# Performance work log

Hardware: AMD Instinct MI355X
Metric: run time of the kernel (lower is better)

The kernel has to match this reference:

```python
import jax, jax.numpy as jnp
import numpy as np

# task -> non-background class ids, padded with -1 to fixed width 3
NBG = np.array([[0, 1, 2], [0, 3, 4], [0, 5, 6], [0, 7, 8],
                [0, 9, -1], [0, 10, -1], [0, 11, -1]], dtype=np.int32)
NEG = -1e9      # pad logit (finite stand-in for -inf, grad-safe)
SMOOTH = 1e-5
NUM_CLASSES = 12


def setup_inputs() -> dict:
    key = jax.random.key(0)
    k1, k2, k3 = jax.random.split(key, 3)
    B, C, D, H, W = 4, 12, 32, 128, 128
    inputs = jax.random.normal(k1, (B, C, D, H, W), dtype=jnp.float32)
    task_id = jax.random.randint(k2, (B,), 0, 7, dtype=jnp.int32)
    # build targets consistent with each sample's task: labels in task_nbg[task]
    raw = jax.random.randint(k3, (B, D, H, W), 0, 3, dtype=jnp.int32)
    nbg = jnp.asarray(NBG)
    ids = nbg[task_id]                                   # [B,3]
    valid_max = jnp.where(ids[:, 2] < 0, 1, 2)           # 2-class tasks: raw in {0,1}
    raw = jnp.minimum(raw, valid_max[:, None, None, None])
    targets = jnp.take_along_axis(ids, raw.reshape(B, -1), axis=1).reshape(B, D, H, W)
    return {"inputs": inputs, "targets": targets, "task_id": task_id}


def reference(inputs, targets, task_id):
    B = inputs.shape[0]
    probs = jax.nn.softmax(inputs, axis=1)               # [B,12,D,H,W]
    nbg = jnp.asarray(NBG)
    ids = nbg[task_id]                                   # [B,3]
    mask = (ids >= 0)                                    # [B,3]
    idsc = jnp.maximum(ids, 0)
    mask5 = mask[:, :, None, None, None]
    gathered = jnp.take_along_axis(probs, idsc[:, :, None, None, None], axis=1)  # [B,3,D,H,W]
    score = jnp.where(mask5, gathered, 0.0)

    # --- remapped marginal targets: labels > 0 shifted by delta ---
    t = task_id.astype(jnp.int32)
    delta = jnp.where(t <= 4, -2 * t, -t - 4)
    tm = jnp.where(targets > 0, targets + delta[:, None, None, None], targets)   # in {0,1,2}

    # --- marginal CE: log_softmax over gathered probs (note: probs, not logits, matching torch F.cross_entropy on softmaxed inputs) ---
    logits = jnp.where(mask5, gathered, NEG)
    logp = jax.nn.log_softmax(logits, axis=1)
    nll = -jnp.take_along_axis(logp, tm[:, None], axis=1)[:, 0]                  # [B,D,H,W]
    loss_marg_ce = nll.mean(axis=(1, 2, 3)).sum() / B

    # --- marginal dice (padded classes contribute exactly 0) ---
    tgt = ((targets[:, None] == idsc[:, :, None, None, None]) & mask5).astype(probs.dtype)
    inter = jnp.sum(score * tgt, axis=(2, 3, 4))
    y_sum = jnp.sum(tgt, axis=(2, 3, 4))                 # tgt is binary: tgt*tgt == tgt
    z_sum = jnp.sum(score * score, axis=(2, 3, 4))
    dice = (2 * inter + SMOOTH) / (z_sum + y_sum + SMOOTH)
    loss_marg_dice = (1.0 - dice).sum() / B

    # --- exclusion: target_e = 1 - onehot(targets, 0..11), class 0 zeroed ---
    cls = jnp.arange(NUM_CLASSES, dtype=targets.dtype)[None, :, None, None, None]
    onehot = (targets[:, None] == cls).astype(probs.dtype)
    te = 1.0 - onehot
    te = te.at[:, 0].set(0.0)
    inter_e = jnp.sum(probs * te, axis=(2, 3, 4))
    y_e = jnp.sum(te, axis=(2, 3, 4))
    z_e = jnp.sum(probs * probs, axis=(2, 3, 4))
    dice_e = (2 * inter_e + SMOOTH) / (z_e + y_e + SMOOTH)
    loss_exc_dice = dice_e.sum() / B                     # inv=True: sum of dice scores

    loss_exc_ce = (jnp.log1p(probs) * te).mean(axis=(2, 3, 4)).sum() / B

    return (loss_marg_dice, loss_marg_ce, loss_exc_dice, loss_exc_ce)
```

## Files before the change

### kernel.cpp

```cpp
#include <hip/hip_runtime.h>


#define S4 131072
#define BLOCKS_PER_B 256
#define THREADS 256
#define NVOX 524288.0f
#define SMOOTH 1e-5f
#define L2E 1.4426950408889634f
#define LN2 0.6931471805599453f

__global__ void zero_acc(float* __restrict__ acc) {
  acc[blockIdx.x * 256 + threadIdx.x] = 0.f;
}

#define TAIL(CM) {                                                             \
  const int tv = tg.CM;                                                        \
  const bool t0 = (tv == 0), t1 = (tv == id1), t2 = (tv == id2);               \
  c1f += t1 ? 1.f : 0.f;  c2f += t2 ? 1.f : 0.f;                               \
  p0S += t0 ? g0.CM : 0.f; p1S += t1 ? g1.CM : 0.f; p2S += t2 ? g2.CM : 0.f;   \
  const float pt = t1 ? g1.CM : (t2 ? g2.CM : 0.f);                            \
  cesE2 += __builtin_amdgcn_logf(prod.CM * __builtin_amdgcn_rcpf(1.f + pt));   \
  const float s3 = __builtin_amdgcn_exp2f(g0.CM * L2E)                         \
                 + __builtin_amdgcn_exp2f(g1.CM * L2E)                         \
                 + __builtin_amdgcn_exp2f(g2.CM * L2E);                        \
  const float gt = t0 ? g0.CM : (t1 ? g1.CM : g2.CM);                          \
  ces2 += __builtin_amdgcn_logf(s3) - gt * L2E;                               \
}

__global__ __launch_bounds__(THREADS, 4)
void marg_main(const float4* __restrict__ inp, const int4* __restrict__ tgtp,
               const int* __restrict__ task_id, float* __restrict__ acc) {
  const int b   = blockIdx.x / BLOCKS_PER_B;
  const int blk = blockIdx.x % BLOCKS_PER_B;
  const int t   = task_id[b];
  const int id1 = (t <= 4) ? 2*t + 1 : t + 5;
  const int id2 = (t <= 3) ? 2*t + 2 : -1;
  const bool v2 = (id2 >= 0);

  const float4* inB = inp  + (size_t)b * 12 * S4;
  const int4*   tgB = tgtp + (size_t)b * S4;

  float aZ[12], aP[12];
  #pragma unroll
  for (int c = 0; c < 12; ++c) { aZ[c] = 0.f; aP[c] = 0.f; }
  float ces2=0.f, cesE2=0.f, c1f=0.f, c2f=0.f, p0S=0.f, p1S=0.f, p2S=0.f;

  #pragma unroll 1
  for (int it = 0; it < 2; ++it) {
    const int s = (blk * 2 + it) * THREADS + (int)threadIdx.x;
    float4 e[12];
    #pragma unroll
    for (int c = 0; c < 12; ++c) e[c] = inB[c * S4 + s];
    const int4 tg = tgB[s];

    #pragma unroll
    for (int c = 0; c < 12; ++c) {
      e[c].x = __builtin_amdgcn_exp2f(e[c].x * L2E);
      e[c].y = __builtin_amdgcn_exp2f(e[c].y * L2E);
      e[c].z = __builtin_amdgcn_exp2f(e[c].z * L2E);
      e[c].w = __builtin_amdgcn_exp2f(e[c].w * L2E);
    }
    float4 es = e[0];
    #pragma unroll
    for (int c = 1; c < 12; ++c) {
      es.x += e[c].x; es.y += e[c].y; es.z += e[c].z; es.w += e[c].w;
    }
    float4 r;
    r.x = __builtin_amdgcn_rcpf(es.x); r.y = __builtin_amdgcn_rcpf(es.y);
    r.z = __builtin_amdgcn_rcpf(es.z); r.w = __builtin_amdgcn_rcpf(es.w);

    float4 prod = make_float4(1.f, 1.f, 1.f, 1.f);
    #pragma unroll
    for (int c = 0; c < 12; ++c) {
      float4 p;
      p.x = e[c].x * r.x; p.y = e[c].y * r.y;
      p.z = e[c].z * r.z; p.w = e[c].w * r.w;
      aZ[c] += (p.x*p.x + p.y*p.y) + (p.z*p.z + p.w*p.w);
      aP[c] += (p.x + p.y) + (p.z + p.w);
      if (c > 0) {
        prod.x = fmaf(prod.x, p.x, prod.x);
        prod.y = fmaf(prod.y, p.y, prod.y);
        prod.z = fmaf(prod.z, p.z, prod.z);
        prod.w = fmaf(prod.w, p.w, prod.w);
      }
    }

    float4 ge1, ge2;
    switch (id1) {
      case 1:  ge1 = e[1];  break;  case 3:  ge1 = e[3];  break;
      case 5:  ge1 = e[5];  break;  case 7:  ge1 = e[7];  break;
      case 9:  ge1 = e[9];  break;  case 10: ge1 = e[10]; break;
      default: ge1 = e[11]; break;
    }
    switch (id2) {
      case 2:  ge2 = e[2];  break;  case 4:  ge2 = e[4];  break;
      case 6:  ge2 = e[6];  break;  case 8:  ge2 = e[8];  break;
      default: ge2 = make_float4(0.f, 0.f, 0.f, 0.f); break;
    }
    float4 g0, g1, g2;
    g0.x = e[0].x * r.x; g0.y = e[0].y * r.y; g0.z = e[0].z * r.z; g0.w = e[0].w * r.w;
    g1.x = ge1.x * r.x;  g1.y = ge1.y * r.y;  g1.z = ge1.z * r.z;  g1.w = ge1.w * r.w;
    g2.x = v2 ? ge2.x * r.x : -1e30f;  g2.y = v2 ? ge2.y * r.y : -1e30f;
    g2.z = v2 ? ge2.z * r.z : -1e30f;  g2.w = v2 ? ge2.w * r.w : -1e30f;

    TAIL(x); TAIL(y); TAIL(z); TAIL(w);
  }

  float vals[32];
  #pragma unroll
  for (int c = 0; c < 12; ++c) { vals[c] = aZ[c]; vals[12 + c] = aP[c]; }
  vals[24] = ces2; vals[25] = cesE2; vals[26] = c1f; vals[27] = c2f;
  vals[28] = p0S;  vals[29] = p1S;   vals[30] = p2S; vals[31] = 0.f;

  __shared__ float red[32][257];
  #pragma unroll
  for (int v = 0; v < 32; ++v) red[v][threadIdx.x] = vals[v];
  __syncthreads();

  const int val = threadIdx.x & 31;
  const int seg = threadIdx.x >> 5;
  const float* row = red[val];
  float ssum = 0.f;
  #pragma unroll
  for (int k = 0; k < 32; ++k) ssum += row[seg * 32 + k];
  ssum += __shfl_down(ssum, 32);
  if ((threadIdx.x & 63) < 32)
    atomicAdd(acc + (((b * 32 + val)) << 4), ssum);
}

__global__ void finalize(const float* __restrict__ acc,
                         const int* __restrict__ task_id,
                         float* __restrict__ out) {
  if (threadIdx.x != 0) return;
  float lmd = 0.f, lmce = 0.f, led = 0.f, lece = 0.f;
  for (int b = 0; b < 4; ++b) {
    const int t   = task_id[b];
    const int id1 = (t <= 4) ? 2*t + 1 : t + 5;
    const int id2 = (t <= 3) ? 2*t + 2 : -1;
    #define A(v) acc[((b * 32 + (v))) << 4]

    lmce += A(24) * LN2 / NVOX;
    lece += A(25) * LN2 / NVOX;

    const float c1 = A(26), c2 = A(27);
    const float y0 = NVOX - c1 - c2;
    const float d0 = (2.f*A(28) + SMOOTH) / (A(0)   + y0 + SMOOTH);
    const float d1 = (2.f*A(29) + SMOOTH) / (A(id1) + c1 + SMOOTH);
    float d2 = 1.f;
    if (id2 >= 0)
      d2 = (2.f*A(30) + SMOOTH) / (A(id2) + c2 + SMOOTH);
    lmd += (1.f - d0) + (1.f - d1) + (1.f - d2);

    led += SMOOTH / (A(0) + SMOOTH);
    for (int c = 1; c < 12; ++c) {
      const float ptc  = (c == id1) ? A(29) : ((c == id2) ? A(30) : 0.f);
      const float cntc = (c == id1) ? c1    : ((c == id2) ? c2    : 0.f);
      const float inter = A(12 + c) - ptc;
      const float ye    = NVOX - cntc;
      led += (2.f*inter + SMOOTH) / (A(c) + ye + SMOOTH);
    }
    #undef A
  }
  out[0] = lmd  * 0.25f;
  out[1] = lmce * 0.25f;
  out[2] = led  * 0.25f;
  out[3] = lece * 0.25f;
}

extern "C" void kernel_launch(void* const* d_in, const int* in_sizes, int n_in,
                              void* d_out, int out_size, void* d_ws, size_t ws_size,
                              hipStream_t stream) {
  const float* inputs  = (const float*)d_in[0];
  const int*   targets = (const int*)d_in[1];
  const int*   task_id = (const int*)d_in[2];
  float* out = (float*)d_out;
  float* acc = (float*)d_ws;

  zero_acc<<<dim3(8), 256, 0, stream>>>(acc);
  marg_main<<<dim3(4 * BLOCKS_PER_B), THREADS, 0, stream>>>(
      (const float4*)inputs, (const int4*)targets, task_id, acc);
  finalize<<<1, 64, 0, stream>>>(acc, task_id, out);
}
```

Baseline: 199.1 us.

## Issue both iterations' loads up front and reduce via wave shuffles

```diff
diff --git a/kernel.cpp b/kernel.cpp
--- a/kernel.cpp
+++ b/kernel.cpp
@@ -8,6 +8,10 @@
 #define SMOOTH 1e-5f
 #define L2E 1.4426950408889634f
 #define LN2 0.6931471805599453f
+
+#define WRED(v) { v += __shfl_down(v,32); v += __shfl_down(v,16); \
+                  v += __shfl_down(v,8);  v += __shfl_down(v,4);  \
+                  v += __shfl_down(v,2);  v += __shfl_down(v,1); }
 
 __global__ void zero_acc(float* __restrict__ acc) {
   acc[blockIdx.x * 256 + threadIdx.x] = 0.f;
@@ -24,10 +28,56 @@
                  + __builtin_amdgcn_exp2f(g1.CM * L2E)                         \
                  + __builtin_amdgcn_exp2f(g2.CM * L2E);                        \
   const float gt = t0 ? g0.CM : (t1 ? g1.CM : g2.CM);                          \
-  ces2 += __builtin_amdgcn_logf(s3) - gt * L2E;                               \
+  ces2 += __builtin_amdgcn_logf(s3) - gt * L2E;                                \
 }
 
-__global__ __launch_bounds__(THREADS, 4)
+#define COMPUTE(E, GE1, GE2, TG) {                                             \
+  _Pragma("unroll")                                                            \
+  for (int c = 0; c < 12; ++c) {                                               \
+    E[c].x = __builtin_amdgcn_exp2f(E[c].x * L2E);                             \
+    E[c].y = __builtin_amdgcn_exp2f(E[c].y * L2E);                             \
+    E[c].z = __builtin_amdgcn_exp2f(E[c].z * L2E);                             \
+    E[c].w = __builtin_amdgcn_exp2f(E[c].w * L2E);                             \
+  }                                                                            \
+  float4 es = E[0];                                                            \
+  _Pragma("unroll")                                                            \
+  for (int c = 1; c < 12; ++c) {                                               \
+    es.x += E[c].x; es.y += E[c].y; es.z += E[c].z; es.w += E[c].w;            \
+  }                                                                            \
+  float4 r;                                                                    \
+  r.x = __builtin_amdgcn_rcpf(es.x); r.y = __builtin_amdgcn_rcpf(es.y);        \
+  r.z = __builtin_amdgcn_rcpf(es.z); r.w = __builtin_amdgcn_rcpf(es.w);        \
+  float4 prod = make_float4(1.f, 1.f, 1.f, 1.f);                               \
+  _Pragma("unroll")                                                            \
+  for (int c = 0; c < 12; ++c) {                                               \
+    float4 p;                                                                  \
+    p.x = E[c].x * r.x; p.y = E[c].y * r.y;                                    \
+    p.z = E[c].z * r.z; p.w = E[c].w * r.w;                                    \
+    aZ[c] += (p.x*p.x + p.y*p.y) + (p.z*p.z + p.w*p.w);                        \
+    aP[c] += (p.x + p.y) + (p.z + p.w);                                        \
+    if (c > 0) {                                                               \
+      prod.x = fmaf(prod.x, p.x, prod.x);                                      \
+      prod.y = fmaf(prod.y, p.y, prod.y);                                      \
+      prod.z = fmaf(prod.z, p.z, prod.z);                                      \
+      prod.w = fmaf(prod.w, p.w, prod.w);                                      \
+    }                                                                          \
+  }                                                                            \
+  float4 g0, g1, g2;                                                           \
+  g0.x = E[0].x * r.x; g0.y = E[0].y * r.y;                                    \
+  g0.z = E[0].z * r.z; g0.w = E[0].w * r.w;                                    \
+  g1.x = __builtin_amdgcn_exp2f(GE1.x * L2E) * r.x;                            \
+  g1.y = __builtin_amdgcn_exp2f(GE1.y * L2E) * r.y;                            \
+  g1.z = __builtin_amdgcn_exp2f(GE1.z * L2E) * r.z;                            \
+  g1.w = __builtin_amdgcn_exp2f(GE1.w * L2E) * r.w;                            \
+  g2.x = v2 ? __builtin_amdgcn_exp2f(GE2.x * L2E) * r.x : -1e30f;              \
+  g2.y = v2 ? __builtin_amdgcn_exp2f(GE2.y * L2E) * r.y : -1e30f;              \
+  g2.z = v2 ? __builtin_amdgcn_exp2f(GE2.z * L2E) * r.z : -1e30f;              \
+  g2.w = v2 ? __builtin_amdgcn_exp2f(GE2.w * L2E) * r.w : -1e30f;              \
+  const int4 tg = TG;                                                          \
+  TAIL(x); TAIL(y); TAIL(z); TAIL(w);                                          \
+}
+
+__global__ __launch_bounds__(THREADS, 2)
 void marg_main(const float4* __restrict__ inp, const int4* __restrict__ tgtp,
                const int* __restrict__ task_id, float* __restrict__ acc) {
   const int b   = blockIdx.x / BLOCKS_PER_B;
@@ -36,6 +86,7 @@
   const int id1 = (t <= 4) ? 2*t + 1 : t + 5;
   const int id2 = (t <= 3) ? 2*t + 2 : -1;
   const bool v2 = (id2 >= 0);
+  const int id2c = v2 ? id2 : 0;
 
   const float4* inB = inp  + (size_t)b * 12 * S4;
   const int4*   tgB = tgtp + (size_t)b * S4;
@@ -45,87 +96,45 @@
   for (int c = 0; c < 12; ++c) { aZ[c] = 0.f; aP[c] = 0.f; }
   float ces2=0.f, cesE2=0.f, c1f=0.f, c2f=0.f, p0S=0.f, p1S=0.f, p2S=0.f;
 
-  #pragma unroll 1
-  for (int it = 0; it < 2; ++it) {
-    const int s = (blk * 2 + it) * THREADS + (int)threadIdx.x;
-    float4 e[12];
+  const int s0 = blk * (2 * THREADS) + (int)threadIdx.x;
+  const int s1 = s0 + THREADS;
+
+  float4 xa[12], xb[12];
+  #pragma unroll
+  for (int c = 0; c < 12; ++c) xa[c] = inB[(size_t)c * S4 + s0];
+  float4 ga1 = inB[(size_t)id1 * S4 + s0];
+  float4 ga2 = inB[(size_t)id2c * S4 + s0];
+  const int4 ta = tgB[s0];
+  #pragma unroll
+  for (int c = 0; c < 12; ++c) xb[c] = inB[(size_t)c * S4 + s1];
+  float4 gb1 = inB[(size_t)id1 * S4 + s1];
+  float4 gb2 = inB[(size_t)id2c * S4 + s1];
+  const int4 tb = tgB[s1];
+
+  COMPUTE(xa, ga1, ga2, ta);
+  COMPUTE(xb, gb1, gb2, tb);
+
+  WRED(ces2); WRED(cesE2); WRED(c1f); WRED(c2f);
+  WRED(p0S);  WRED(p1S);   WRED(p2S);
+  #pragma unroll
+  for (int c = 0; c < 12; ++c) { WRED(aZ[c]); WRED(aP[c]); }
+
+  __shared__ float red[4][32];
+  const int lane = threadIdx.x & 63;
+  const int wv   = threadIdx.x >> 6;
+  if (lane == 0) {
+    float* rw = red[wv];
     #pragma unroll
-    for (int c = 0; c < 12; ++c) e[c] = inB[c * S4 + s];
-    const int4 tg = tgB[s];
-
-    #pragma unroll
-    for (int c = 0; c < 12; ++c) {
-      e[c].x = __builtin_amdgcn_exp2f(e[c].x * L2E);
-      e[c].y = __builtin_amdgcn_exp2f(e[c].y * L2E);
-      e[c].z = __builtin_amdgcn_exp2f(e[c].z * L2E);
-      e[c].w = __builtin_amdgcn_exp2f(e[c].w * L2E);
-    }
-    float4 es = e[0];
-    #pragma unroll
-    for (int c = 1; c < 12; ++c) {
-      es.x += e[c].x; es.y += e[c].y; es.z += e[c].z; es.w += e[c].w;
-    }
-    float4 r;
-    r.x = __builtin_amdgcn_rcpf(es.x); r.y = __builtin_amdgcn_rcpf(es.y);
-    r.z = __builtin_amdgcn_rcpf(es.z); r.w = __builtin_amdgcn_rcpf(es.w);
-
-    float4 prod = make_float4(1.f, 1.f, 1.f, 1.f);
-    #pragma unroll
-    for (int c = 0; c < 12; ++c) {
-      float4 p;
-      p.x = e[c].x * r.x; p.y = e[c].y * r.y;
-      p.z = e[c].z * r.z; p.w = e[c].w * r.w;
-      aZ[c] += (p.x*p.x + p.y*p.y) + (p.z*p.z + p.w*p.w);
-      aP[c] += (p.x + p.y) + (p.z + p.w);
-      if (c > 0) {
-        prod.x = fmaf(prod.x, p.x, prod.x);
-        prod.y = fmaf(prod.y, p.y, prod.y);
-        prod.z = fmaf(prod.z, p.z, prod.z);
-        prod.w = fmaf(prod.w, p.w, prod.w);
-      }
-    }
-
-    float4 ge1, ge2;
-    switch (id1) {
-      case 1:  ge1 = e[1];  break;  case 3:  ge1 = e[3];  break;
-      case 5:  ge1 = e[5];  break;  case 7:  ge1 = e[7];  break;
-      case 9:  ge1 = e[9];  break;  case 10: ge1 = e[10]; break;
-      default: ge1 = e[11]; break;
-    }
-    switch (id2) {
-      case 2:  ge2 = e[2];  break;  case 4:  ge2 = e[4];  break;
-      case 6:  ge2 = e[6];  break;  case 8:  ge2 = e[8];  break;
-      default: ge2 = make_float4(0.f, 0.f, 0.f, 0.f); break;
-    }
-    float4 g0, g1, g2;
-    g0.x = e[0].x * r.x; g0.y = e[0].y * r.y; g0.z = e[0].z * r.z; g0.w = e[0].w * r.w;
-    g1.x = ge1.x * r.x;  g1.y = ge1.y * r.y;  g1.z = ge1.z * r.z;  g1.w = ge1.w * r.w;
-    g2.x = v2 ? ge2.x * r.x : -1e30f;  g2.y = v2 ? ge2.y * r.y : -1e30f;
-    g2.z = v2 ? ge2.z * r.z : -1e30f;  g2.w = v2 ? ge2.w * r.w : -1e30f;
-
-    TAIL(x); TAIL(y); TAIL(z); TAIL(w);
+    for (int c = 0; c < 12; ++c) { rw[c] = aZ[c]; rw[12 + c] = aP[c]; }
+    rw[24] = ces2; rw[25] = cesE2; rw[26] = c1f; rw[27] = c2f;
+    rw[28] = p0S;  rw[29] = p1S;   rw[30] = p2S; rw[31] = 0.f;
   }
-
-  float vals[32];
-  #pragma unroll
-  for (int c = 0; c < 12; ++c) { vals[c] = aZ[c]; vals[12 + c] = aP[c]; }
-  vals[24] = ces2; vals[25] = cesE2; vals[26] = c1f; vals[27] = c2f;
-  vals[28] = p0S;  vals[29] = p1S;   vals[30] = p2S; vals[31] = 0.f;
-
-  __shared__ float red[32][257];
-  #pragma unroll
-  for (int v = 0; v < 32; ++v) red[v][threadIdx.x] = vals[v];
   __syncthreads();
-
-  const int val = threadIdx.x & 31;
-  const int seg = threadIdx.x >> 5;
-  const float* row = red[val];
-  float ssum = 0.f;
-  #pragma unroll
-  for (int k = 0; k < 32; ++k) ssum += row[seg * 32 + k];
-  ssum += __shfl_down(ssum, 32);
-  if ((threadIdx.x & 63) < 32)
-    atomicAdd(acc + (((b * 32 + val)) << 4), ssum);
+  if (threadIdx.x < 32) {
+    const float sv = red[0][threadIdx.x] + red[1][threadIdx.x]
+                   + red[2][threadIdx.x] + red[3][threadIdx.x];
+    atomicAdd(acc + ((b * 32 + (int)threadIdx.x) << 4), sv);
+  }
 }
 
 __global__ void finalize(const float* __restrict__ acc,
```

Result: faster. 181.8 us (-8.7%).

## Stage logits through LDS via global_load_lds and use wave-shuffle reductions

Applied to the files above, without the earlier changes.

```diff
diff --git a/kernel.cpp b/kernel.cpp
--- a/kernel.cpp
+++ b/kernel.cpp
@@ -4,13 +4,24 @@
 #define S4 131072
 #define BLOCKS_PER_B 256
 #define THREADS 256
+#define TILES_PER_BLOCK 2
 #define NVOX 524288.0f
 #define SMOOTH 1e-5f
 #define L2E 1.4426950408889634f
 #define LN2 0.6931471805599453f
 
+#define WRED(v) { v += __shfl_down(v,32); v += __shfl_down(v,16); \
+                  v += __shfl_down(v,8);  v += __shfl_down(v,4);  \
+                  v += __shfl_down(v,2);  v += __shfl_down(v,1); }
+
 __global__ void zero_acc(float* __restrict__ acc) {
   acc[blockIdx.x * 256 + threadIdx.x] = 0.f;
+}
+
+__device__ __forceinline__ void gload_lds16(const float4* g, float4* ldsbase) {
+  __builtin_amdgcn_global_load_lds(
+      (const __attribute__((address_space(1))) void*)g,
+      (__attribute__((address_space(3))) void*)ldsbase, 16, 0, 0);
 }
 
 #define TAIL(CM) {                                                             \
@@ -24,18 +35,25 @@
                  + __builtin_amdgcn_exp2f(g1.CM * L2E)                         \
                  + __builtin_amdgcn_exp2f(g2.CM * L2E);                        \
   const float gt = t0 ? g0.CM : (t1 ? g1.CM : g2.CM);                          \
-  ces2 += __builtin_amdgcn_logf(s3) - gt * L2E;                               \
-}
-
-__global__ __launch_bounds__(THREADS, 4)
+  ces2 += __builtin_amdgcn_logf(s3) - gt * L2E;                                \
+}
+
+__global__ __launch_bounds__(THREADS, 3)
 void marg_main(const float4* __restrict__ inp, const int4* __restrict__ tgtp,
                const int* __restrict__ task_id, float* __restrict__ acc) {
-  const int b   = blockIdx.x / BLOCKS_PER_B;
-  const int blk = blockIdx.x % BLOCKS_PER_B;
-  const int t   = task_id[b];
-  const int id1 = (t <= 4) ? 2*t + 1 : t + 5;
-  const int id2 = (t <= 3) ? 2*t + 2 : -1;
-  const bool v2 = (id2 >= 0);
+  __shared__ float4 ldsA[12][THREADS];
+  __shared__ float red[4][32];
+
+  const int b    = blockIdx.x / BLOCKS_PER_B;
+  const int blk  = blockIdx.x % BLOCKS_PER_B;
+  const int tid  = threadIdx.x;
+  const int wv   = tid >> 6;
+  const int lane = tid & 63;
+  const int t    = task_id[b];
+  const int id1  = (t <= 4) ? 2*t + 1 : t + 5;
+  const int id2  = (t <= 3) ? 2*t + 2 : -1;
+  const bool v2  = (id2 >= 0);
+  const int id2c = v2 ? id2 : 0;
 
   const float4* inB = inp  + (size_t)b * 12 * S4;
   const int4*   tgB = tgtp + (size_t)b * S4;
@@ -46,24 +64,28 @@
   float ces2=0.f, cesE2=0.f, c1f=0.f, c2f=0.f, p0S=0.f, p1S=0.f, p2S=0.f;
 
   #pragma unroll 1
-  for (int it = 0; it < 2; ++it) {
-    const int s = (blk * 2 + it) * THREADS + (int)threadIdx.x;
-    float4 e[12];
-    #pragma unroll
-    for (int c = 0; c < 12; ++c) e[c] = inB[c * S4 + s];
-    const int4 tg = tgB[s];
-
+  for (int it = 0; it < TILES_PER_BLOCK; ++it) {
+    const int g0i = (blk * TILES_PER_BLOCK + it) * THREADS;
+
+    #pragma unroll
+    for (int c = 0; c < 12; ++c)
+      gload_lds16(&inB[(size_t)c * S4 + g0i + tid], &ldsA[c][wv << 6]);
+    const int4 tg = tgB[g0i + tid];
+    __syncthreads();
+
+    float4 xv[12];
     #pragma unroll
     for (int c = 0; c < 12; ++c) {
-      e[c].x = __builtin_amdgcn_exp2f(e[c].x * L2E);
-      e[c].y = __builtin_amdgcn_exp2f(e[c].y * L2E);
-      e[c].z = __builtin_amdgcn_exp2f(e[c].z * L2E);
-      e[c].w = __builtin_amdgcn_exp2f(e[c].w * L2E);
-    }
-    float4 es = e[0];
+      const float4 v = ldsA[c][tid];
+      xv[c].x = __builtin_amdgcn_exp2f(v.x * L2E);
+      xv[c].y = __builtin_amdgcn_exp2f(v.y * L2E);
+      xv[c].z = __builtin_amdgcn_exp2f(v.z * L2E);
+      xv[c].w = __builtin_amdgcn_exp2f(v.w * L2E);
+    }
+    float4 es = xv[0];
     #pragma unroll
     for (int c = 1; c < 12; ++c) {
-      es.x += e[c].x; es.y += e[c].y; es.z += e[c].z; es.w += e[c].w;
+      es.x += xv[c].x; es.y += xv[c].y; es.z += xv[c].z; es.w += xv[c].w;
     }
     float4 r;
     r.x = __builtin_amdgcn_rcpf(es.x); r.y = __builtin_amdgcn_rcpf(es.y);
@@ -73,8 +95,8 @@
     #pragma unroll
     for (int c = 0; c < 12; ++c) {
       float4 p;
-      p.x = e[c].x * r.x; p.y = e[c].y * r.y;
-      p.z = e[c].z * r.z; p.w = e[c].w * r.w;
+      p.x = xv[c].x * r.x; p.y = xv[c].y * r.y;
+      p.z = xv[c].z * r.z; p.w = xv[c].w * r.w;
       aZ[c] += (p.x*p.x + p.y*p.y) + (p.z*p.z + p.w*p.w);
       aP[c] += (p.x + p.y) + (p.z + p.w);
       if (c > 0) {
@@ -85,47 +107,42 @@
       }
     }
 
-    float4 ge1, ge2;
-    switch (id1) {
-      case 1:  ge1 = e[1];  break;  case 3:  ge1 = e[3];  break;
-      case 5:  ge1 = e[5];  break;  case 7:  ge1 = e[7];  break;
-      case 9:  ge1 = e[9];  break;  case 10: ge1 = e[10]; break;
-      default: ge1 = e[11]; break;
-    }
-    switch (id2) {
-      case 2:  ge2 = e[2];  break;  case 4:  ge2 = e[4];  break;
-      case 6:  ge2 = e[6];  break;  case 8:  ge2 = e[8];  break;
-      default: ge2 = make_float4(0.f, 0.f, 0.f, 0.f); break;
-    }
+    const float4 v1 = ldsA[id1][tid];
+    const float4 vv2 = ldsA[id2c][tid];
     float4 g0, g1, g2;
-    g0.x = e[0].x * r.x; g0.y = e[0].y * r.y; g0.z = e[0].z * r.z; g0.w = e[0].w * r.w;
-    g1.x = ge1.x * r.x;  g1.y = ge1.y * r.y;  g1.z = ge1.z * r.z;  g1.w = ge1.w * r.w;
-    g2.x = v2 ? ge2.x * r.x : -1e30f;  g2.y = v2 ? ge2.y * r.y : -1e30f;
-    g2.z = v2 ? ge2.z * r.z : -1e30f;  g2.w = v2 ? ge2.w * r.w : -1e30f;
+    g0.x = xv[0].x * r.x; g0.y = xv[0].y * r.y;
+    g0.z = xv[0].z * r.z; g0.w = xv[0].w * r.w;
+    g1.x = __builtin_amdgcn_exp2f(v1.x * L2E) * r.x;
+    g1.y = __builtin_amdgcn_exp2f(v1.y * L2E) * r.y;
+    g1.z = __builtin_amdgcn_exp2f(v1.z * L2E) * r.z;
+    g1.w = __builtin_amdgcn_exp2f(v1.w * L2E) * r.w;
+    g2.x = v2 ? __builtin_amdgcn_exp2f(vv2.x * L2E) * r.x : -1e30f;
+    g2.y = v2 ? __builtin_amdgcn_exp2f(vv2.y * L2E) * r.y : -1e30f;
+    g2.z = v2 ? __builtin_amdgcn_exp2f(vv2.z * L2E) * r.z : -1e30f;
+    g2.w = v2 ? __builtin_amdgcn_exp2f(vv2.w * L2E) * r.w : -1e30f;
 
     TAIL(x); TAIL(y); TAIL(z); TAIL(w);
-  }
-
-  float vals[32];
+
+    __syncthreads();
+  }
+
+  WRED(ces2); WRED(cesE2); WRED(c1f); WRED(c2f);
+  WRED(p0S);  WRED(p1S);   WRED(p2S);
   #pragma unroll
-  for (int c = 0; c < 12; ++c) { vals[c] = aZ[c]; vals[12 + c] = aP[c]; }
-  vals[24] = ces2; vals[25] = cesE2; vals[26] = c1f; vals[27] = c2f;
-  vals[28] = p0S;  vals[29] = p1S;   vals[30] = p2S; vals[31] = 0.f;
-
-  __shared__ float red[32][257];
-  #pragma unroll
-  for (int v = 0; v < 32; ++v) red[v][threadIdx.x] = vals[v];
+  for (int c = 0; c < 12; ++c) { WRED(aZ[c]); WRED(aP[c]); }
+
+  if (lane == 0) {
+    float* rw = red[wv];
+    #pragma unroll
+    for (int c = 0; c < 12; ++c) { rw[c] = aZ[c]; rw[12 + c] = aP[c]; }
+    rw[24] = ces2; rw[25] = cesE2; rw[26] = c1f; rw[27] = c2f;
+    rw[28] = p0S;  rw[29] = p1S;   rw[30] = p2S; rw[31] = 0.f;
+  }
   __syncthreads();
-
-  const int val = threadIdx.x & 31;
-  const int seg = threadIdx.x >> 5;
-  const float* row = red[val];
-  float ssum = 0.f;
-  #pragma unroll
-  for (int k = 0; k < 32; ++k) ssum += row[seg * 32 + k];
-  ssum += __shfl_down(ssum, 32);
-  if ((threadIdx.x & 63) < 32)
-    atomicAdd(acc + (((b * 32 + val)) << 4), ssum);
+  if (tid < 32) {
+    const float sv = red[0][tid] + red[1][tid] + red[2][tid] + red[3][tid];
+    atomicAdd(acc + ((b * 32 + tid) << 4), sv);
+  }
 }
 
 __global__ void finalize(const float* __restrict__ acc,
```

Measured after the change: 172.5 us. 1.15x faster.

## Drop per-thread loop, double grid, use wave-shuffle reduction with small LDS

Applied to the files above, without the earlier changes.

```diff
diff --git a/kernel.cpp b/kernel.cpp
--- a/kernel.cpp
+++ b/kernel.cpp
@@ -2,12 +2,16 @@
 
 
 #define S4 131072
-#define BLOCKS_PER_B 256
+#define BLOCKS_PER_B 512
 #define THREADS 256
 #define NVOX 524288.0f
 #define SMOOTH 1e-5f
 #define L2E 1.4426950408889634f
 #define LN2 0.6931471805599453f
+
+#define WRED(v) { v += __shfl_down(v,32); v += __shfl_down(v,16); \
+                  v += __shfl_down(v,8);  v += __shfl_down(v,4);  \
+                  v += __shfl_down(v,2);  v += __shfl_down(v,1); }
 
 __global__ void zero_acc(float* __restrict__ acc) {
   acc[blockIdx.x * 256 + threadIdx.x] = 0.f;
@@ -24,14 +28,15 @@
                  + __builtin_amdgcn_exp2f(g1.CM * L2E)                         \
                  + __builtin_amdgcn_exp2f(g2.CM * L2E);                        \
   const float gt = t0 ? g0.CM : (t1 ? g1.CM : g2.CM);                          \
-  ces2 += __builtin_amdgcn_logf(s3) - gt * L2E;                               \
+  ces2 += __builtin_amdgcn_logf(s3) - gt * L2E;                                \
 }
 
-__global__ __launch_bounds__(THREADS, 4)
+__global__ __launch_bounds__(THREADS, 8)
 void marg_main(const float4* __restrict__ inp, const int4* __restrict__ tgtp,
                const int* __restrict__ task_id, float* __restrict__ acc) {
-  const int b   = blockIdx.x / BLOCKS_PER_B;
-  const int blk = blockIdx.x % BLOCKS_PER_B;
+  const int b   = blockIdx.x >> 9;
+  const int blk = blockIdx.x & 511;
+  const int tid = threadIdx.x;
   const int t   = task_id[b];
   const int id1 = (t <= 4) ? 2*t + 1 : t + 5;
   const int id2 = (t <= 3) ? 2*t + 2 : -1;
@@ -39,93 +44,81 @@
 
   const float4* inB = inp  + (size_t)b * 12 * S4;
   const int4*   tgB = tgtp + (size_t)b * S4;
+  const int g = blk * THREADS + tid;
+
+  float4 e[12];
+  #pragma unroll
+  for (int c = 0; c < 12; ++c) e[c] = inB[(size_t)c * S4 + g];
+  const int4 tg = tgB[g];
+
+  #pragma unroll
+  for (int c = 0; c < 12; ++c) {
+    e[c].x = __builtin_amdgcn_exp2f(e[c].x * L2E);
+    e[c].y = __builtin_amdgcn_exp2f(e[c].y * L2E);
+    e[c].z = __builtin_amdgcn_exp2f(e[c].z * L2E);
+    e[c].w = __builtin_amdgcn_exp2f(e[c].w * L2E);
+  }
+  float4 es = e[0];
+  #pragma unroll
+  for (int c = 1; c < 12; ++c) {
+    es.x += e[c].x; es.y += e[c].y; es.z += e[c].z; es.w += e[c].w;
+  }
+  float4 r;
+  r.x = __builtin_amdgcn_rcpf(es.x); r.y = __builtin_amdgcn_rcpf(es.y);
+  r.z = __builtin_amdgcn_rcpf(es.z); r.w = __builtin_amdgcn_rcpf(es.w);
 
   float aZ[12], aP[12];
+  float4 prod = make_float4(1.f, 1.f, 1.f, 1.f);
+  float4 g0, g1, g2;
+  g1 = make_float4(0.f, 0.f, 0.f, 0.f);
+  g2 = make_float4(0.f, 0.f, 0.f, 0.f);
   #pragma unroll
-  for (int c = 0; c < 12; ++c) { aZ[c] = 0.f; aP[c] = 0.f; }
+  for (int c = 0; c < 12; ++c) {
+    float4 p;
+    p.x = e[c].x * r.x; p.y = e[c].y * r.y;
+    p.z = e[c].z * r.z; p.w = e[c].w * r.w;
+    aZ[c] = (p.x*p.x + p.y*p.y) + (p.z*p.z + p.w*p.w);
+    aP[c] = (p.x + p.y) + (p.z + p.w);
+    if (c == 0) {
+      g0 = p;
+    } else {
+      prod.x = fmaf(prod.x, p.x, prod.x);
+      prod.y = fmaf(prod.y, p.y, prod.y);
+      prod.z = fmaf(prod.z, p.z, prod.z);
+      prod.w = fmaf(prod.w, p.w, prod.w);
+      const bool m1 = (c == id1);
+      g1.x = m1 ? p.x : g1.x; g1.y = m1 ? p.y : g1.y;
+      g1.z = m1 ? p.z : g1.z; g1.w = m1 ? p.w : g1.w;
+      const bool m2 = (c == id2);
+      g2.x = m2 ? p.x : g2.x; g2.y = m2 ? p.y : g2.y;
+      g2.z = m2 ? p.z : g2.z; g2.w = m2 ? p.w : g2.w;
+    }
+  }
+  if (!v2) g2 = make_float4(-1e30f, -1e30f, -1e30f, -1e30f);
+
   float ces2=0.f, cesE2=0.f, c1f=0.f, c2f=0.f, p0S=0.f, p1S=0.f, p2S=0.f;
+  TAIL(x); TAIL(y); TAIL(z); TAIL(w);
 
-  #pragma unroll 1
-  for (int it = 0; it < 2; ++it) {
-    const int s = (blk * 2 + it) * THREADS + (int)threadIdx.x;
-    float4 e[12];
+  WRED(ces2); WRED(cesE2); WRED(c1f); WRED(c2f);
+  WRED(p0S);  WRED(p1S);   WRED(p2S);
+  #pragma unroll
+  for (int c = 0; c < 12; ++c) { WRED(aZ[c]); WRED(aP[c]); }
+
+  __shared__ float red[4][32];
+  const int lane = tid & 63;
+  const int wv   = tid >> 6;
+  if (lane == 0) {
+    float* rw = red[wv];
     #pragma unroll
-    for (int c = 0; c < 12; ++c) e[c] = inB[c * S4 + s];
-    const int4 tg = tgB[s];
-
-    #pragma unroll
-    for (int c = 0; c < 12; ++c) {
-      e[c].x = __builtin_amdgcn_exp2f(e[c].x * L2E);
-      e[c].y = __builtin_amdgcn_exp2f(e[c].y * L2E);
-      e[c].z = __builtin_amdgcn_exp2f(e[c].z * L2E);
-      e[c].w = __builtin_amdgcn_exp2f(e[c].w * L2E);
-    }
-    float4 es = e[0];
-    #pragma unroll
-    for (int c = 1; c < 12; ++c) {
-      es.x += e[c].x; es.y += e[c].y; es.z += e[c].z; es.w += e[c].w;
-    }
-    float4 r;
-    r.x = __builtin_amdgcn_rcpf(es.x); r.y = __builtin_amdgcn_rcpf(es.y);
-    r.z = __builtin_amdgcn_rcpf(es.z); r.w = __builtin_amdgcn_rcpf(es.w);
-
-    float4 prod = make_float4(1.f, 1.f, 1.f, 1.f);
-    #pragma unroll
-    for (int c = 0; c < 12; ++c) {
-      float4 p;
-      p.x = e[c].x * r.x; p.y = e[c].y * r.y;
-      p.z = e[c].z * r.z; p.w = e[c].w * r.w;
-      aZ[c] += (p.x*p.x + p.y*p.y) + (p.z*p.z + p.w*p.w);
-      aP[c] += (p.x + p.y) + (p.z + p.w);
-      if (c > 0) {
-        prod.x = fmaf(prod.x, p.x, prod.x);
-        prod.y = fmaf(prod.y, p.y, prod.y);
-        prod.z = fmaf(prod.z, p.z, prod.z);
-        prod.w = fmaf(prod.w, p.w, prod.w);
-      }
-    }
-
-    float4 ge1, ge2;
-    switch (id1) {
-      case 1:  ge1 = e[1];  break;  case 3:  ge1 = e[3];  break;
-      case 5:  ge1 = e[5];  break;  case 7:  ge1 = e[7];  break;
-      case 9:  ge1 = e[9];  break;  case 10: ge1 = e[10]; break;
-      default: ge1 = e[11]; break;
-    }
-    switch (id2) {
-      case 2:  ge2 = e[2];  break;  case 4:  ge2 = e[4];  break;
-      case 6:  ge2 = e[6];  break;  case 8:  ge2 = e[8];  break;
-      default: ge2 = make_float4(0.f, 0.f, 0.f, 0.f); break;
-    }
-    float4 g0, g1, g2;
-    g0.x = e[0].x * r.x; g0.y = e[0].y * r.y; g0.z = e[0].z * r.z; g0.w = e[0].w * r.w;
-    g1.x = ge1.x * r.x;  g1.y = ge1.y * r.y;  g1.z = ge1.z * r.z;  g1.w = ge1.w * r.w;
-    g2.x = v2 ? ge2.x * r.x : -1e30f;  g2.y = v2 ? ge2.y * r.y : -1e30f;
-    g2.z = v2 ? ge2.z * r.z : -1e30f;  g2.w = v2 ? ge2.w * r.w : -1e30f;
-
-    TAIL(x); TAIL(y); TAIL(z); TAIL(w);
+    for (int c = 0; c < 12; ++c) { rw[c] = aZ[c]; rw[12 + c] = aP[c]; }
+    rw[24] = ces2; rw[25] = cesE2; rw[26] = c1f; rw[27] = c2f;
+    rw[28] = p0S;  rw[29] = p1S;   rw[30] = p2S; rw[31] = 0.f;
   }
-
-  float vals[32];
-  #pragma unroll
-  for (int c = 0; c < 12; ++c) { vals[c] = aZ[c]; vals[12 + c] = aP[c]; }
-  vals[24] = ces2; vals[25] = cesE2; vals[26] = c1f; vals[27] = c2f;
-  vals[28] = p0S;  vals[29] = p1S;   vals[30] = p2S; vals[31] = 0.f;
-
-  __shared__ float red[32][257];
-  #pragma unroll
-  for (int v = 0; v < 32; ++v) red[v][threadIdx.x] = vals[v];
   __syncthreads();
-
-  const int val = threadIdx.x & 31;
-  const int seg = threadIdx.x >> 5;
-  const float* row = red[val];
-  float ssum = 0.f;
-  #pragma unroll
-  for (int k = 0; k < 32; ++k) ssum += row[seg * 32 + k];
-  ssum += __shfl_down(ssum, 32);
-  if ((threadIdx.x & 63) < 32)
-    atomicAdd(acc + (((b * 32 + val)) << 4), ssum);
+  if (tid < 32) {
+    const float sv = red[0][tid] + red[1][tid] + red[2][tid] + red[3][tid];
+    atomicAdd(acc + ((b * 32 + tid) << 4), sv);
+  }
 }
 
 __global__ void finalize(const float* __restrict__ acc,
```

New measurement: 194.6 us. -2.3%, faster.
